# Kernel optimization log

Measured on AMD Instinct MI355X. Metric: run time of the kernel, lower is better.

The kernel has to match this reference:

```python
import jax, jax.numpy as jnp
import numpy as np

GRID_SIZE = 5
SPLINE_ORDER = 3
NUM_COEFF = GRID_SIZE + SPLINE_ORDER  # 8
L = 3
B, I, H = 4096, 256, 512
EPS = 1e-5


def make_grid(in_features):
    # efficient-kan default grid over [-1, 1] extended by spline_order knots each side
    h = 2.0 / GRID_SIZE
    g = jnp.arange(-SPLINE_ORDER, GRID_SIZE + SPLINE_ORDER + 1, dtype=jnp.float32) * h - 1.0
    return jnp.broadcast_to(g, (in_features, g.shape[0]))  # (in, G+2k+1)


def b_splines(x, grid):
    # x: (B, in), grid: (in, G+2k+1) -> (B, in, G+k) via Cox-de-Boor recursion
    xg = x[..., None]
    bases = ((xg >= grid[:, :-1]) & (xg < grid[:, 1:])).astype(x.dtype)
    for j in range(1, SPLINE_ORDER + 1):
        left = (xg - grid[:, :-(j + 1)]) / (grid[:, j:-1] - grid[:, :-(j + 1)])
        right = (grid[:, j + 1:] - xg) / (grid[:, j + 1:] - grid[:, 1:-j])
        bases = left * bases[..., :-1] + right * bases[..., 1:]
    return bases


def kan_linear(x, base_w, spline_w, grid):
    # base path: SiLU(x) @ W_base^T ; spline path: sum over (in, coeff)
    base = jax.nn.silu(x) @ base_w.T
    spl = jnp.einsum('bik,oik->bo', b_splines(x, grid), spline_w)
    return base + spl


def layer_norm(x, g, b):
    mu = jnp.mean(x, axis=-1, keepdims=True)
    var = jnp.var(x, axis=-1, keepdims=True)
    return (x - mu) / jnp.sqrt(var + EPS) * g + b


def _sublayer(z_prev, wx_b, wx_s, wh_b, wh_s, hz_b, hz_s, phi_b, phi_s,
              hh_w, hh_b, ln_g, ln_b, x_t, grid_in, grid_h):
    s_t = kan_linear(x_t, wx_b, wx_s, grid_in) + kan_linear(z_prev, wh_b, wh_s, grid_h)
    o_t = kan_linear(s_t, phi_b, phi_s, grid_h)
    z_t = layer_norm(z_prev @ hh_w.T + hh_b + kan_linear(o_t, hz_b, hz_s, grid_h), ln_g, ln_b)
    return o_t, z_t


def setup_inputs() -> dict:
    key = jax.random.key(0)
    ks = jax.random.split(key, 24)
    s = 0.05  # small init to keep gates/splines in sane range
    inp = {
        'x_t': jax.random.normal(ks[0], (B, I), jnp.float32),
        'h_prev': jax.random.normal(ks[1], (B, H), jnp.float32),
        'c_prev': jax.random.normal(ks[2], (B, H), jnp.float32),
        'z_prev': jax.random.normal(ks[3], (L, B, H), jnp.float32),
        'wx_base': jax.random.normal(ks[4], (L, H, I), jnp.float32) * s,
        'wx_spline': jax.random.normal(ks[5], (L, H, I, NUM_COEFF), jnp.float32) * s,
        'wh_base': jax.random.normal(ks[6], (L, H, H), jnp.float32) * s,
        'wh_spline': jax.random.normal(ks[7], (L, H, H, NUM_COEFF), jnp.float32) * s,
        'hz_base': jax.random.normal(ks[8], (L, H, H), jnp.float32) * s,
        'hz_spline': jax.random.normal(ks[9], (L, H, H, NUM_COEFF), jnp.float32) * s,
        'phi_base': jax.random.normal(ks[10], (L, H, H), jnp.float32) * s,
        'phi_spline': jax.random.normal(ks[11], (L, H, H, NUM_COEFF), jnp.float32) * s,
        'hh_w': jax.random.normal(ks[12], (L, H, H), jnp.float32) * s,
        'hh_b': jax.random.normal(ks[13], (L, H), jnp.float32) * s,
        'ln_g': jnp.ones((L, H), jnp.float32),
        'ln_b': jnp.zeros((L, H), jnp.float32),
        'f_w': jax.random.normal(ks[14], (H, I + H), jnp.float32) * s,
        'f_b': jax.random.normal(ks[15], (H,), jnp.float32) * s,
        'i_w': jax.random.normal(ks[16], (H, I + H), jnp.float32) * s,
        'i_b': jax.random.normal(ks[17], (H,), jnp.float32) * s,
        'g_w': jax.random.normal(ks[18], (H, I + H), jnp.float32) * s,
        'g_b': jax.random.normal(ks[19], (H,), jnp.float32) * s,
        'o_w': jax.random.normal(ks[20], (H, L * H), jnp.float32) * s,
        'o_b': jax.random.normal(ks[21], (H,), jnp.float32) * s,
    }
    return inp


def reference(x_t, h_prev, c_prev, z_prev, wx_base, wx_spline, wh_base, wh_spline,
              hz_base, hz_spline, phi_base, phi_spline, hh_w, hh_b, ln_g, ln_b,
              f_w, f_b, i_w, i_b, g_w, g_b, o_w, o_b):
    grid_in = make_grid(I)
    grid_h = make_grid(H)
    cat = jnp.concatenate([x_t, h_prev], axis=-1)  # (B, I+H)
    f_t = jax.nn.sigmoid(cat @ f_w.T + f_b)
    i_t = jax.nn.sigmoid(cat @ i_w.T + i_b)
    g_t = jnp.tanh(cat @ g_w.T + g_b)
    # vmap the RKAN sublayer over the L stacked sublayers
    sub = jax.vmap(_sublayer, in_axes=(0,) * 13 + (None, None, None))
    o_all, z_all = sub(z_prev, wx_base, wx_spline, wh_base, wh_spline,
                       hz_base, hz_spline, phi_base, phi_spline,
                       hh_w, hh_b, ln_g, ln_b, x_t, grid_in, grid_h)
    # concat sublayer phi outputs: (L,B,H) -> (B, L*H)
    r_t = jnp.transpose(o_all, (1, 0, 2)).reshape(B, L * H)
    o_t = jax.nn.sigmoid(r_t @ o_w.T + o_b)
    c_t = f_t * c_prev + i_t * g_t
    h_t = o_t * jnp.tanh(c_t)
    return h_t, c_t, z_all
```

## Files before the change

kernel.cpp:

```cpp
#include <hip/hip_runtime.h>

typedef __attribute__((ext_vector_type(8))) short short8;
typedef __attribute__((ext_vector_type(4))) float floatx4;

__device__ inline short f2bf(float v) {
    unsigned u = __builtin_bit_cast(unsigned, v);
    unsigned r = (u + 0x7fffu + ((u >> 16) & 1u)) >> 16;
    return (short)r;
}
__device__ inline float bf2f(short s) {
    unsigned u = ((unsigned)(unsigned short)s) << 16;
    return __builtin_bit_cast(float, u);
}

__device__ inline void spline8(float v, short* arr) {
    float u = (v + 2.2f) * 2.5f;
    float fj = floorf(u);
    int jj = (int)fj;
    float t1 = u - fj;
    float ok = (jj >= 0 && jj <= 10) ? (1.f / 6.f) : 0.f;
    float t2 = t1 * t1, t3 = t2 * t1;
    float omt = 1.f - t1;
    short sw0 = f2bf(omt * omt * omt * ok);
    short sw1 = f2bf((3.f * t3 - 6.f * t2 + 4.f) * ok);
    short sw2 = f2bf((-3.f * t3 + 3.f * t2 + 3.f * t1 + 1.f) * ok);
    short sw3 = f2bf(t3 * ok);
#pragma unroll
    for (int s = 0; s < 8; ++s) {
        int rr = s - jj + 3;
        arr[s] = (rr == 0) ? sw0 : (rr == 1) ? sw1 : (rr == 2) ? sw2
                 : (rr == 3) ? sw3 : (short)0;
    }
}

__global__ __launch_bounds__(512, 4) void gemm256(
    int S, int Kh,
    const short* __restrict__ A0, int lda0, long sA0, int K0,
    const short* __restrict__ W0, int ldw0, long sW0,
    const short* __restrict__ A1, int lda1, long sA1, int K1,
    const short* __restrict__ W1, int ldw1, long sW1,
    float* __restrict__ C, int ldc, long sC, long sSplit)
{
    __shared__ short As[256 * 32];
    __shared__ short Ws[128 * 32];
    const int t = threadIdx.x;
    int n = blockIdx.x + (blockIdx.y << 4) + (blockIdx.z << 6);
    int k8 = n & 7, j = n >> 3;
    int byi = j & 3;
    int bxi = (k8 << 1) + ((j >> 2) & 1);
    int bzi = j >> 3;
    const int z = bzi / S, s = bzi % S;
    const int bm = bxi * 256, bn = byi * 128;
    const int lane = t & 63, w = t >> 6;
    const int wm = (w >> 1) * 64, wn = (w & 1) * 64;
    const int lrow = lane & 15, quad = lane >> 4;

    floatx4 acc[4][4] = {};

    const int kbeg = s * Kh, kend = kbeg + Kh;

    const short* A = A0 + (long)z * sA0;
    const short* W = W0 + (long)z * sW0;
    int lda = lda0, ldw = ldw0;
    int kb = kbeg, ke = (kend < K0) ? kend : K0;

    for (int seg = 0; seg < 2; ++seg) {
        for (int kv = kb; kv < ke; kv += 32) {
#pragma unroll
            for (int i = 0; i < 2; ++i) {
                int c = i * 512 + t;
                int row = c >> 2, cg = (c & 3) * 8;
                const short* gp = A + (long)(bm + row) * lda + kv + cg;
                __builtin_amdgcn_global_load_lds(
                    (const __attribute__((address_space(1))) void*)gp,
                    (__attribute__((address_space(3))) void*)(As + c * 8), 16, 0, 0);
            }
            {
                int row = t >> 2, cg = (t & 3) * 8;
                const short* gq = W + (long)(bn + row) * ldw + kv + cg;
                __builtin_amdgcn_global_load_lds(
                    (const __attribute__((address_space(1))) void*)gq,
                    (__attribute__((address_space(3))) void*)(Ws + t * 8), 16, 0, 0);
            }
            __syncthreads();
            short8 af[4], bfr[4];
#pragma unroll
            for (int mi = 0; mi < 4; ++mi)
                af[mi] = *(const short8*)(As + (wm + mi * 16 + lrow) * 32 + quad * 8);
#pragma unroll
            for (int ni = 0; ni < 4; ++ni)
                bfr[ni] = *(const short8*)(Ws + (wn + ni * 16 + lrow) * 32 + quad * 8);
#pragma unroll
            for (int mi = 0; mi < 4; ++mi)
#pragma unroll
                for (int ni = 0; ni < 4; ++ni)
                    acc[mi][ni] = __builtin_amdgcn_mfma_f32_16x16x32_bf16(
                        af[mi], bfr[ni], acc[mi][ni], 0, 0, 0);
            __syncthreads();
        }
        A = A1 + (long)z * sA1;
        W = W1 + (long)z * sW1;
        lda = lda1; ldw = ldw1;
        kb = ((kbeg > K0) ? kbeg : K0) - K0;
        ke = kend - K0;
    }

    float* Cz = C + (long)z * sC + (long)s * sSplit;
#pragma unroll
    for (int mi = 0; mi < 4; ++mi)
#pragma unroll
        for (int ni = 0; ni < 4; ++ni)
#pragma unroll
            for (int r = 0; r < 4; ++r) {
                int row = bm + wm + mi * 16 + quad * 4 + r;
                int col = bn + wn + ni * 16 + lrow;
                Cz[(long)row * ldc + col] = acc[mi][ni][r];
            }
}

__global__ __launch_bounds__(256) void gemm64(
    int swz,
    const short* __restrict__ A0, int lda0, long sA0, int K0,
    const short* __restrict__ W0, int ldw0, long sW0,
    const short* __restrict__ A1, int lda1, long sA1, int K1,
    const short* __restrict__ W1, int ldw1, long sW1,
    short* __restrict__ C, int ldc, long sC)
{
    __shared__ short As[64 * 32];
    __shared__ short Ws[128 * 32];
    const int t = threadIdx.x;
    int bxi = blockIdx.x, byi = blockIdx.y, bzi = blockIdx.z;
    if (swz) {
        int n = bxi + (byi << 6) + (bzi << 8);
        int k = n & 7, j = n >> 3;
        byi = j & 3;
        bxi = k * 8 + ((j >> 2) & 7);
        bzi = j >> 5;
    }
    const int z = bzi;
    const int bm = bxi * 64;
    const int bn = byi * 128;
    const int lane = t & 63, w = t >> 6;
    const int wm = (w >> 1) * 32, wn = (w & 1) * 64;
    const int lrow = lane & 15, quad = lane >> 4;

    floatx4 acc[2][4] = {};

    const short* A = A0 + (long)z * sA0;
    const short* W = W0 + (long)z * sW0;
    int K = K0, lda = lda0, ldw = ldw0;

    for (int seg = 0; seg < 2; ++seg) {
        for (int k0 = 0; k0 < K; k0 += 32) {
            {
                int row = t >> 2, cg = (t & 3) * 8;
                const short* gp = A + (long)(bm + row) * lda + k0 + cg;
                __builtin_amdgcn_global_load_lds(
                    (const __attribute__((address_space(1))) void*)gp,
                    (__attribute__((address_space(3))) void*)(As + t * 8), 16, 0, 0);
            }
#pragma unroll
            for (int j = 0; j < 2; ++j) {
                int cj = j * 256 + t;
                int row = cj >> 2, cg = (cj & 3) * 8;
                const short* gq = W + (long)(bn + row) * ldw + k0 + cg;
                __builtin_amdgcn_global_load_lds(
                    (const __attribute__((address_space(1))) void*)gq,
                    (__attribute__((address_space(3))) void*)(Ws + cj * 8), 16, 0, 0);
            }
            __syncthreads();
            short8 af[2], bfr[4];
#pragma unroll
            for (int mi = 0; mi < 2; ++mi)
                af[mi] = *(const short8*)(As + (wm + mi * 16 + lrow) * 32 + quad * 8);
#pragma unroll
            for (int ni = 0; ni < 4; ++ni)
                bfr[ni] = *(const short8*)(Ws + (wn + ni * 16 + lrow) * 32 + quad * 8);
#pragma unroll
            for (int mi = 0; mi < 2; ++mi)
#pragma unroll
                for (int ni = 0; ni < 4; ++ni)
                    acc[mi][ni] = __builtin_amdgcn_mfma_f32_16x16x32_bf16(
                        af[mi], bfr[ni], acc[mi][ni], 0, 0, 0);
            __syncthreads();
        }
        A = A1 + (long)z * sA1; W = W1 + (long)z * sW1;
        K = K1; lda = lda1; ldw = ldw1;
    }

    short* Cz = C + (long)z * sC;
#pragma unroll
    for (int mi = 0; mi < 2; ++mi)
#pragma unroll
        for (int ni = 0; ni < 4; ++ni)
#pragma unroll
            for (int r = 0; r < 4; ++r) {
                int row = bm + wm + mi * 16 + quad * 4 + r;
                int col = bn + wn + ni * 16 + lrow;
                Cz[(long)row * ldc + col] = f2bf(acc[mi][ni][r]);
            }
}

__global__ __launch_bounds__(256) void megapack4(
    const float* __restrict__ wx_b, const float* __restrict__ wx_s,
    const float* __restrict__ wh_b, const float* __restrict__ wh_s,
    const float* __restrict__ hz_b, const float* __restrict__ hz_s,
    const float* __restrict__ phi_b, const float* __restrict__ phi_s,
    const float* __restrict__ hh_w, const float* __restrict__ o_w,
    const float* __restrict__ f_w, const float* __restrict__ i_w,
    const float* __restrict__ g_w,
    short* __restrict__ Wx, short* __restrict__ Wh, short* __restrict__ Whz,
    short* __restrict__ Wphi, short* __restrict__ HHb, short* __restrict__ OWb,
    short* __restrict__ Wg)
{
    int bid = blockIdx.x, tid = threadIdx.x;
    float4 v;
    short* dst;
    long e;
    if (bid < 3456) {
        e = ((long)bid * 256 + tid) * 4;
        int r = (int)(e / 2304), c = (int)(e % 2304);
        v = (c < 256) ? *(const float4*)(wx_b + (long)r * 256 + c)
                      : *(const float4*)(wx_s + (long)r * 2048 + (c - 256));
        dst = Wx + e;
    } else if (bid < 24192) {
        int jb = bid - 3456;
        int job = jb / 6912, lb = jb % 6912;
        const float* bp = (job == 0) ? wh_b : (job == 1) ? hz_b : phi_b;
        const float* sp = (job == 0) ? wh_s : (job == 1) ? hz_s : phi_s;
        short* dp = (job == 0) ? Wh : (job == 1) ? Whz : Wphi;
        e = ((long)lb * 256 + tid) * 4;
        int r = (int)(e / 4608), c = (int)(e % 4608);
        v = (c < 512) ? *(const float4*)(bp + (long)r * 512 + c)
                      : *(const float4*)(sp + (long)r * 4096 + (c - 512));
        dst = dp + e;
    } else if (bid < 24960) {
        e = ((long)(bid - 24192) * 256 + tid) * 4;
        v = *(const float4*)(hh_w + e);
        dst = HHb + e;
    } else if (bid < 25728) {
        e = ((long)(bid - 24960) * 256 + tid) * 4;
        v = *(const float4*)(o_w + e);
        dst = OWb + e;
    } else if (bid < 26112) {
        e = ((long)(bid - 25728) * 256 + tid) * 4;
        v = *(const float4*)(f_w + e);
        dst = Wg + e;
    } else if (bid < 26496) {
        e = ((long)(bid - 26112) * 256 + tid) * 4;
        v = *(const float4*)(i_w + e);
        dst = Wg + 393216 + e;
    } else {
        e = ((long)(bid - 26496) * 256 + tid) * 4;
        v = *(const float4*)(g_w + e);
        dst = Wg + 786432 + e;
    }
    dst[0] = f2bf(v.x); dst[1] = f2bf(v.y);
    dst[2] = f2bf(v.z); dst[3] = f2bf(v.w);
}

__global__ __launch_bounds__(256) void prep_acts(
    const float* __restrict__ x_t, const float* __restrict__ h_prev,
    const float* __restrict__ z_prev,
    short* __restrict__ Xe, short* __restrict__ Agate,
    short* __restrict__ Ze, short* __restrict__ zraw)
{
    int bid = blockIdx.x, tid = threadIdx.x;
    if (bid < 4096) {
        int r = bid, i = tid;
        float v = x_t[(long)r * 256 + i];
        Agate[(long)r * 768 + i] = f2bf(v);
        long ob = (long)r * 2304;
        Xe[ob + i] = f2bf(v / (1.f + __expf(-v)));
        short arr[8];
        spline8(v, arr);
        *(short8*)(Xe + ob + 256 + (long)i * 8) = *(const short8*)arr;
    } else if (bid < 12288) {
        long idx = (long)(bid - 4096) * 256 + tid;
        long b = idx >> 9; int hh = (int)(idx & 511);
        Agate[b * 768 + 256 + hh] = f2bf(h_prev[idx]);
    } else {
        int j = bid - 12288;
        int r = j >> 1, i = (j & 1) * 256 + tid;
        float v = z_prev[(long)r * 512 + i];
        zraw[(long)r * 512 + i] = f2bf(v);
        long ob = (long)r * 4608;
        Ze[ob + i] = f2bf(v / (1.f + __expf(-v)));
        short arr[8];
        spline8(v, arr);
        *(short8*)(Ze + ob + 512 + (long)i * 8) = *(const short8*)arr;
    }
}

__global__ __launch_bounds__(256) void expand_pair(
    const float* __restrict__ P, long sSplit, int S, int inF,
    short* __restrict__ out, short* __restrict__ compact)
{
    int i = (blockIdx.x * 256 + threadIdx.x) * 2;
    int r = blockIdx.y;
    long idx = (long)r * inF + i;
    float2 v = *(const float2*)(P + idx);
    for (int s = 1; s < S; ++s) {
        float2 a = *(const float2*)(P + idx + (long)s * sSplit);
        v.x += a.x; v.y += a.y;
    }
    if (compact) { compact[idx] = f2bf(v.x); compact[idx + 1] = f2bf(v.y); }

    long ob = (long)r * inF * 9;
    out[ob + i]     = f2bf(v.x / (1.f + __expf(-v.x)));
    out[ob + i + 1] = f2bf(v.y / (1.f + __expf(-v.y)));

    short arr[8];
    spline8(v.x, arr);
    *(short8*)(out + ob + inF + (long)i * 8) = *(const short8*)arr;
    spline8(v.y, arr);
    *(short8*)(out + ob + inF + (long)(i + 1) * 8) = *(const short8*)arr;
}

__global__ __launch_bounds__(256) void ln_pair(const float* __restrict__ P,
                                               long sSplit, int S,
                                               const float* __restrict__ hh_b,
                                               const float* __restrict__ ln_g,
                                               const float* __restrict__ ln_b,
                                               float* __restrict__ out)
{
    int row = blockIdx.x;
    int l = row >> 12;
    int t = threadIdx.x;
    long base = (long)row * 512;
    float v0 = hh_b[l * 512 + t];
    float v1 = hh_b[l * 512 + t + 256];
    for (int s = 0; s < S; ++s) {
        v0 += P[base + t + (long)s * sSplit];
        v1 += P[base + t + 256 + (long)s * sSplit];
    }
    float sm = v0 + v1, sq = v0 * v0 + v1 * v1;
#pragma unroll
    for (int off = 32; off; off >>= 1) {
        sm += __shfl_down(sm, off);
        sq += __shfl_down(sq, off);
    }
    __shared__ float ls[4], lq[4];
    int w = t >> 6, lane = t & 63;
    if (lane == 0) { ls[w] = sm; lq[w] = sq; }
    __syncthreads();
    float Sm = ls[0] + ls[1] + ls[2] + ls[3];
    float Q = lq[0] + lq[1] + lq[2] + lq[3];
    float mu = Sm * (1.f / 512.f);
    float var = Q * (1.f / 512.f) - mu * mu;
    float rstd = rsqrtf(var + 1e-5f);
    float* o = out + (long)row * 512;
    o[t]       = (v0 - mu) * rstd * ln_g[l * 512 + t]       + ln_b[l * 512 + t];
    o[t + 256] = (v1 - mu) * rstd * ln_g[l * 512 + t + 256] + ln_b[l * 512 + t + 256];
}

__global__ __launch_bounds__(256) void cell_epilogue(const short* __restrict__ gates,
                                                     const short* __restrict__ opre,
                                                     const float* __restrict__ c_prev,
                                                     const float* __restrict__ f_b,
                                                     const float* __restrict__ i_b,
                                                     const float* __restrict__ g_b,
                                                     const float* __restrict__ o_b,
                                                     float* __restrict__ out)
{
    long idx = blockIdx.x * 256L + threadIdx.x;
    long b = idx >> 9; int h = (int)(idx & 511);
    const short* g = gates + b * 1536;
    float fp = bf2f(g[h]) + f_b[h];
    float ip = bf2f(g[512 + h]) + i_b[h];
    float gp = bf2f(g[1024 + h]) + g_b[h];
    float op = bf2f(opre[idx]) + o_b[h];
    float ft = 1.f / (1.f + __expf(-fp));
    float it = 1.f / (1.f + __expf(-ip));
    float gt = tanhf(gp);
    float ot = 1.f / (1.f + __expf(-op));
    float c = ft * c_prev[idx] + it * gt;
    out[idx] = ot * tanhf(c);
    out[idx + 2097152] = c;
}

extern "C" void kernel_launch(void* const* d_in, const int* in_sizes, int n_in,
                              void* d_out, int out_size, void* d_ws, size_t ws_size,
                              hipStream_t stream)
{
    const float* x_t       = (const float*)d_in[0];
    const float* h_prev    = (const float*)d_in[1];
    const float* c_prev    = (const float*)d_in[2];
    const float* z_prev    = (const float*)d_in[3];
    const float* wx_base   = (const float*)d_in[4];
    const float* wx_spline = (const float*)d_in[5];
    const float* wh_base   = (const float*)d_in[6];
    const float* wh_spline = (const float*)d_in[7];
    const float* hz_base   = (const float*)d_in[8];
    const float* hz_spline = (const float*)d_in[9];
    const float* phi_base  = (const float*)d_in[10];
    const float* phi_spline= (const float*)d_in[11];
    const float* hh_w      = (const float*)d_in[12];
    const float* hh_b      = (const float*)d_in[13];
    const float* ln_g      = (const float*)d_in[14];
    const float* ln_b      = (const float*)d_in[15];
    const float* f_w       = (const float*)d_in[16];
    const float* f_b       = (const float*)d_in[17];
    const float* i_w       = (const float*)d_in[18];
    const float* i_b       = (const float*)d_in[19];
    const float* g_w       = (const float*)d_in[20];
    const float* g_b       = (const float*)d_in[21];
    const float* o_w       = (const float*)d_in[22];
    const float* o_b       = (const float*)d_in[23];
    float* out = (float*)d_out;
    const long BH = 4096L * 512;

    char* p = (char*)d_ws;
    auto alloc = [&](size_t bytes) {
        char* q = p;
        p += (bytes + 255) & ~(size_t)255;
        return q;
    };

    short* Wx   = (short*)alloc(3L * 512 * 2304 * 2);
    short* Wh   = (short*)alloc(3L * 512 * 4608 * 2);
    short* Whz  = (short*)alloc(3L * 512 * 4608 * 2);
    short* Wphi = (short*)alloc(3L * 512 * 4608 * 2);
    short* HHb  = (short*)alloc(3L * 512 * 512 * 2);
    short* OWb  = (short*)alloc(512L * 1536 * 2);
    short* Wg   = (short*)alloc(1536L * 768 * 2);
    short* Agate= (short*)alloc(4096L * 768 * 2);
    short* zraw = (short*)alloc(3L * 4096 * 512 * 2);
    short* XR   = (short*)alloc(4096L * 2304 * 2);
    short* Ebuf = (short*)alloc(3L * 4096 * 4608 * 2);

    const long PS = 3L * 4096 * 512;
    size_t used = (size_t)(p - (char*)d_ws);
    size_t splitB = (size_t)PS * 4;
    int S = (ws_size >= used + 4 * splitB + 4096) ? 4 : 2;
    float* Pbuf = (float*)alloc((size_t)S * splitB);

    short* Xe = XR;
    short* Rbuf = XR;
    short* gbuf = Ebuf;
    short* opre = Ebuf + 4096L * 1536;

    megapack4<<<26880, 256, 0, stream>>>(
        wx_base, wx_spline, wh_base, wh_spline, hz_base, hz_spline,
        phi_base, phi_spline, hh_w, o_w, f_w, i_w, g_w,
        Wx, Wh, Whz, Wphi, HHb, OWb, Wg);

    prep_acts<<<36864, 256, 0, stream>>>(x_t, h_prev, z_prev, Xe, Agate, Ebuf, zraw);

    gemm256<<<dim3(16, 4, 3 * S), 512, 0, stream>>>(S, 6912 / S,
        Xe, 2304, 0, 2304,                 Wx, 2304, 512L * 2304,
        Ebuf, 4608, 4096L * 4608, 4608,    Wh, 4608, 512L * 4608,
        Pbuf, 512, 4096L * 512, PS);

    expand_pair<<<dim3(1, 12288), 256, 0, stream>>>(Pbuf, PS, S, 512, Ebuf, (short*)0);

    gemm256<<<dim3(16, 4, 3 * S), 512, 0, stream>>>(S, 4608 / S,
        Ebuf, 4608, 4096L * 4608, 4608,    Wphi, 4608, 512L * 4608,
        zraw, 0, 0, 0,                     Wphi, 0, 0,
        Pbuf, 1536, 512, PS);

    expand_pair<<<dim3(1, 12288), 256, 0, stream>>>(Pbuf, PS, S, 512, Ebuf, Rbuf);

    gemm256<<<dim3(16, 4, 3 * S), 512, 0, stream>>>(S, 5120 / S,
        Ebuf, 13824, 4608, 4608,           Whz, 4608, 512L * 4608,
        zraw, 512, 4096L * 512, 512,       HHb, 512, 512L * 512,
        Pbuf, 512, 4096L * 512, PS);

    ln_pair<<<12288, 256, 0, stream>>>(Pbuf, PS, S, hh_b, ln_g, ln_b, out + 2 * BH);

    gemm64<<<dim3(64, 12, 1), 256, 0, stream>>>(0,
        Agate, 768, 0, 768,  Wg, 768, 0,
        Agate, 768, 0, 0,    Wg, 768, 0,
        gbuf, 1536, 0);

    gemm64<<<dim3(64, 4, 1), 256, 0, stream>>>(0,
        Rbuf, 1536, 0, 1536, OWb, 1536, 0,
        Rbuf, 1536, 0, 0,    OWb, 1536, 0,
        opre, 512, 0);

    cell_epilogue<<<8192, 256, 0, stream>>>(gbuf, opre, c_prev, f_b, i_b, g_b, o_b, out);
}
```

Baseline: 770.2 us.

## Retile split-K GEMM to 128x128 with BK=64 swizzled LDS and fix split count

```diff
diff --git a/kernel.cpp b/kernel.cpp
--- a/kernel.cpp
+++ b/kernel.cpp
@@ -33,7 +33,7 @@
     }
 }
 
-__global__ __launch_bounds__(512, 4) void gemm256(
+__global__ __launch_bounds__(256, 3) void gemm128(
     int S, int Kh,
     const short* __restrict__ A0, int lda0, long sA0, int K0,
     const short* __restrict__ W0, int ldw0, long sW0,
@@ -41,16 +41,17 @@
     const short* __restrict__ W1, int ldw1, long sW1,
     float* __restrict__ C, int ldc, long sC, long sSplit)
 {
-    __shared__ short As[256 * 32];
-    __shared__ short Ws[128 * 32];
+    __shared__ short As[128 * 64];
+    __shared__ short Ws[128 * 64];
     const int t = threadIdx.x;
-    int n = blockIdx.x + (blockIdx.y << 4) + (blockIdx.z << 6);
+    int n = blockIdx.x + (blockIdx.y << 5) + (blockIdx.z << 7);
     int k8 = n & 7, j = n >> 3;
     int byi = j & 3;
-    int bxi = (k8 << 1) + ((j >> 2) & 1);
-    int bzi = j >> 3;
+    int t2 = j >> 2;
+    int bxi = k8 * 4 + (t2 & 3);
+    int bzi = t2 >> 2;
     const int z = bzi / S, s = bzi % S;
-    const int bm = bxi * 256, bn = byi * 128;
+    const int bm = bxi * 128, bn = byi * 128;
     const int lane = t & 63, w = t >> 6;
     const int wm = (w >> 1) * 64, wn = (w & 1) * 64;
     const int lrow = lane & 15, quad = lane >> 4;
@@ -65,37 +66,44 @@
     int kb = kbeg, ke = (kend < K0) ? kend : K0;
 
     for (int seg = 0; seg < 2; ++seg) {
-        for (int kv = kb; kv < ke; kv += 32) {
-#pragma unroll
-            for (int i = 0; i < 2; ++i) {
-                int c = i * 512 + t;
-                int row = c >> 2, cg = (c & 3) * 8;
+        for (int kv = kb; kv < ke; kv += 64) {
+#pragma unroll
+            for (int i = 0; i < 4; ++i) {
+                int c = i * 256 + t;
+                int row = c >> 3;
+                int cg = ((c ^ row) & 7) * 8;
                 const short* gp = A + (long)(bm + row) * lda + kv + cg;
                 __builtin_amdgcn_global_load_lds(
                     (const __attribute__((address_space(1))) void*)gp,
                     (__attribute__((address_space(3))) void*)(As + c * 8), 16, 0, 0);
-            }
-            {
-                int row = t >> 2, cg = (t & 3) * 8;
                 const short* gq = W + (long)(bn + row) * ldw + kv + cg;
                 __builtin_amdgcn_global_load_lds(
                     (const __attribute__((address_space(1))) void*)gq,
-                    (__attribute__((address_space(3))) void*)(Ws + t * 8), 16, 0, 0);
+                    (__attribute__((address_space(3))) void*)(Ws + c * 8), 16, 0, 0);
             }
             __syncthreads();
-            short8 af[4], bfr[4];
-#pragma unroll
-            for (int mi = 0; mi < 4; ++mi)
-                af[mi] = *(const short8*)(As + (wm + mi * 16 + lrow) * 32 + quad * 8);
-#pragma unroll
-            for (int ni = 0; ni < 4; ++ni)
-                bfr[ni] = *(const short8*)(Ws + (wn + ni * 16 + lrow) * 32 + quad * 8);
-#pragma unroll
-            for (int mi = 0; mi < 4; ++mi)
-#pragma unroll
-                for (int ni = 0; ni < 4; ++ni)
-                    acc[mi][ni] = __builtin_amdgcn_mfma_f32_16x16x32_bf16(
-                        af[mi], bfr[ni], acc[mi][ni], 0, 0, 0);
+#pragma unroll
+            for (int kk = 0; kk < 2; ++kk) {
+                short8 af[4], bfr[4];
+#pragma unroll
+                for (int mi = 0; mi < 4; ++mi) {
+                    int r = wm + mi * 16 + lrow;
+                    af[mi] = *(const short8*)(As + r * 64 +
+                                              (((kk * 4 + quad) ^ (r & 7)) * 8));
+                }
+#pragma unroll
+                for (int ni = 0; ni < 4; ++ni) {
+                    int r = wn + ni * 16 + lrow;
+                    bfr[ni] = *(const short8*)(Ws + r * 64 +
+                                               (((kk * 4 + quad) ^ (r & 7)) * 8));
+                }
+#pragma unroll
+                for (int mi = 0; mi < 4; ++mi)
+#pragma unroll
+                    for (int ni = 0; ni < 4; ++ni)
+                        acc[mi][ni] = __builtin_amdgcn_mfma_f32_16x16x32_bf16(
+                            af[mi], bfr[ni], acc[mi][ni], 0, 0, 0);
+            }
             __syncthreads();
         }
         A = A1 + (long)z * sA1;
@@ -317,41 +325,47 @@
     *(short8*)(out + ob + inF + (long)(i + 1) * 8) = *(const short8*)arr;
 }
 
-__global__ __launch_bounds__(256) void ln_pair(const float* __restrict__ P,
+__global__ __launch_bounds__(256) void ln_wave(const float* __restrict__ P,
                                                long sSplit, int S,
                                                const float* __restrict__ hh_b,
                                                const float* __restrict__ ln_g,
                                                const float* __restrict__ ln_b,
                                                float* __restrict__ out)
 {
-    int row = blockIdx.x;
+    int wv = threadIdx.x >> 6, lane = threadIdx.x & 63;
+    int row = blockIdx.x * 4 + wv;
     int l = row >> 12;
-    int t = threadIdx.x;
-    long base = (long)row * 512;
-    float v0 = hh_b[l * 512 + t];
-    float v1 = hh_b[l * 512 + t + 256];
+    int col = lane * 8;
+    long base = (long)row * 512 + col;
+    float v[8];
+#pragma unroll
+    for (int e = 0; e < 8; ++e) v[e] = hh_b[l * 512 + col + e];
     for (int s = 0; s < S; ++s) {
-        v0 += P[base + t + (long)s * sSplit];
-        v1 += P[base + t + 256 + (long)s * sSplit];
-    }
-    float sm = v0 + v1, sq = v0 * v0 + v1 * v1;
+        float4 a = *(const float4*)(P + base + (long)s * sSplit);
+        float4 b = *(const float4*)(P + base + 4 + (long)s * sSplit);
+        v[0] += a.x; v[1] += a.y; v[2] += a.z; v[3] += a.w;
+        v[4] += b.x; v[5] += b.y; v[6] += b.z; v[7] += b.w;
+    }
+    float sm = 0.f, sq = 0.f;
+#pragma unroll
+    for (int e = 0; e < 8; ++e) { sm += v[e]; sq += v[e] * v[e]; }
 #pragma unroll
     for (int off = 32; off; off >>= 1) {
         sm += __shfl_down(sm, off);
         sq += __shfl_down(sq, off);
     }
-    __shared__ float ls[4], lq[4];
-    int w = t >> 6, lane = t & 63;
-    if (lane == 0) { ls[w] = sm; lq[w] = sq; }
-    __syncthreads();
-    float Sm = ls[0] + ls[1] + ls[2] + ls[3];
-    float Q = lq[0] + lq[1] + lq[2] + lq[3];
-    float mu = Sm * (1.f / 512.f);
-    float var = Q * (1.f / 512.f) - mu * mu;
+    sm = __shfl(sm, 0);
+    sq = __shfl(sq, 0);
+    float mu = sm * (1.f / 512.f);
+    float var = sq * (1.f / 512.f) - mu * mu;
     float rstd = rsqrtf(var + 1e-5f);
-    float* o = out + (long)row * 512;
-    o[t]       = (v0 - mu) * rstd * ln_g[l * 512 + t]       + ln_b[l * 512 + t];
-    o[t + 256] = (v1 - mu) * rstd * ln_g[l * 512 + t + 256] + ln_b[l * 512 + t + 256];
+    float o[8];
+#pragma unroll
+    for (int e = 0; e < 8; ++e)
+        o[e] = (v[e] - mu) * rstd * ln_g[l * 512 + col + e] + ln_b[l * 512 + col + e];
+    float* op = out + base;
+    *(float4*)op = make_float4(o[0], o[1], o[2], o[3]);
+    *(float4*)(op + 4) = make_float4(o[4], o[5], o[6], o[7]);
 }
 
 __global__ __launch_bounds__(256) void cell_epilogue(const short* __restrict__ gates,
@@ -429,11 +443,9 @@
     short* XR   = (short*)alloc(4096L * 2304 * 2);
     short* Ebuf = (short*)alloc(3L * 4096 * 4608 * 2);
 
+    const int S = 2;
     const long PS = 3L * 4096 * 512;
-    size_t used = (size_t)(p - (char*)d_ws);
-    size_t splitB = (size_t)PS * 4;
-    int S = (ws_size >= used + 4 * splitB + 4096) ? 4 : 2;
-    float* Pbuf = (float*)alloc((size_t)S * splitB);
+    float* Pbuf = (float*)alloc((size_t)S * PS * 4);
 
     short* Xe = XR;
     short* Rbuf = XR;
@@ -447,26 +459,26 @@
 
     prep_acts<<<36864, 256, 0, stream>>>(x_t, h_prev, z_prev, Xe, Agate, Ebuf, zraw);
 
-    gemm256<<<dim3(16, 4, 3 * S), 512, 0, stream>>>(S, 6912 / S,
+    gemm128<<<dim3(32, 4, 3 * S), 256, 0, stream>>>(S, 3456,
         Xe, 2304, 0, 2304,                 Wx, 2304, 512L * 2304,
         Ebuf, 4608, 4096L * 4608, 4608,    Wh, 4608, 512L * 4608,
         Pbuf, 512, 4096L * 512, PS);
 
     expand_pair<<<dim3(1, 12288), 256, 0, stream>>>(Pbuf, PS, S, 512, Ebuf, (short*)0);
 
-    gemm256<<<dim3(16, 4, 3 * S), 512, 0, stream>>>(S, 4608 / S,
+    gemm128<<<dim3(32, 4, 3 * S), 256, 0, stream>>>(S, 2304,
         Ebuf, 4608, 4096L * 4608, 4608,    Wphi, 4608, 512L * 4608,
         zraw, 0, 0, 0,                     Wphi, 0, 0,
         Pbuf, 1536, 512, PS);
 
     expand_pair<<<dim3(1, 12288), 256, 0, stream>>>(Pbuf, PS, S, 512, Ebuf, Rbuf);
 
-    gemm256<<<dim3(16, 4, 3 * S), 512, 0, stream>>>(S, 5120 / S,
+    gemm128<<<dim3(32, 4, 3 * S), 256, 0, stream>>>(S, 2560,
         Ebuf, 13824, 4608, 4608,           Whz, 4608, 512L * 4608,
         zraw, 512, 4096L * 512, 512,       HHb, 512, 512L * 512,
         Pbuf, 512, 4096L * 512, PS);
 
-    ln_pair<<<12288, 256, 0, stream>>>(Pbuf, PS, S, hh_b, ln_g, ln_b, out + 2 * BH);
+    ln_wave<<<3072, 256, 0, stream>>>(Pbuf, PS, S, hh_b, ln_g, ln_b, out + 2 * BH);
 
     gemm64<<<dim3(64, 12, 1), 256, 0, stream>>>(0,
         Agate, 768, 0, 768,  Wg, 768, 0,
```

Result: faster. 695.5 us (-9.7%).
